# Kernel optimization log

Measured on AMD Instinct MI355X. Metric: run time of the kernel, lower is better.

## Reference

```python
import jax, jax.numpy as jnp
import numpy as np

B, S, D = 16, 2048, 64
SCALE = 1.0 / np.sqrt(np.float32(D))  # forward divides by sqrt(embedding_dim=64)


def setup_inputs() -> dict:
    key = jax.random.key(0)
    ks = jax.random.split(key, 7)
    return {
        "x": jax.random.normal(ks[0], (B, S, D), dtype=jnp.float32),
        "Wq": jax.random.normal(ks[1], (D, D), dtype=jnp.float32) * 0.02,
        "bq": jax.random.normal(ks[2], (D,), dtype=jnp.float32) * 0.02,
        "Wk": jax.random.normal(ks[3], (D, D), dtype=jnp.float32) * 0.02,
        "bk": jax.random.normal(ks[4], (D,), dtype=jnp.float32) * 0.02,
        "Wv": jax.random.normal(ks[5], (D, D), dtype=jnp.float32) * 0.02,
        "bv": jax.random.normal(ks[6], (D,), dtype=jnp.float32) * 0.02,
    }


def reference(x, Wq, bq, Wk, bk, Wv, bv):
    # Linear projections (weights stored [in, out], math-equivalent to nn.Linear)
    q = jnp.einsum("bsd,de->bse", x, Wq) + bq
    k = jnp.einsum("bsd,de->bse", x, Wk) + bk
    v = jnp.einsum("bsd,de->bse", x, Wv) + bv
    # Unfused scores: [B, S, S]
    scores = jnp.einsum("bqd,bkd->bqk", q, k) * jnp.float32(SCALE)
    causal = jnp.tril(jnp.ones((S, S), dtype=bool))  # mask[:S,:S]
    scores = jnp.where(causal, scores, jnp.float32(-jnp.inf))
    attn = jax.nn.softmax(scores, axis=-1)
    # dropout is identity in eval mode (reference baseline)
    out = jnp.einsum("bqk,bkd->bqd", attn, v)
    return out
```

## Files before the change

### kernel.cpp

```cpp
#include <hip/hip_runtime.h>

#define NB 16
#define SS 2048
#define DD 64

typedef __attribute__((ext_vector_type(8))) short short8;
typedef __attribute__((ext_vector_type(4))) float f32x4;

#define SCL2E 0.18033688011112042f

__device__ __forceinline__ short f2bf(float f) {
  union { float f; unsigned u; } v; v.f = f;
  unsigned r = (v.u + 0x7fffu + ((v.u >> 16) & 1u)) >> 16;
  return (short)r;
}

__device__ __forceinline__ unsigned cvtpk_bf16(float lo, float hi) {
  unsigned r;
  asm("v_cvt_pk_bf16_f32 %0, %1, %2" : "=v"(r) : "v"(lo), "v"(hi));
  return r;
}

__device__ __forceinline__ short8 load_a_frag_f32(const float* p) {
  float4 u = *(const float4*)p;
  float4 w = *(const float4*)(p + 4);
  short8 r;
  r[0] = f2bf(u.x); r[1] = f2bf(u.y); r[2] = f2bf(u.z); r[3] = f2bf(u.w);
  r[4] = f2bf(w.x); r[5] = f2bf(w.y); r[6] = f2bf(w.z); r[7] = f2bf(w.w);
  return r;
}

__global__ __launch_bounds__(256) void wprep_kernel(
    const float* __restrict__ Wq, const float* __restrict__ Wk,
    const float* __restrict__ Wv, ushort* __restrict__ Wt)
{
  const float* Ws[3] = {Wq, Wk, Wv};
  const int m = blockIdx.x;
  const float* src = Ws[m];
  ushort* dst = Wt + m * 4096;
  const int t = threadIdx.x;
#pragma unroll
  for (int i = 0; i < 4; ++i) {
    int idx = i * 1024 + t * 4;
    int k = idx >> 6, n0 = idx & 63;
    float4 w4 = *(const float4*)(src + idx);
    dst[(n0 + 0) * 64 + k] = (ushort)f2bf(w4.x);
    dst[(n0 + 1) * 64 + k] = (ushort)f2bf(w4.y);
    dst[(n0 + 2) * 64 + k] = (ushort)f2bf(w4.z);
    dst[(n0 + 3) * 64 + k] = (ushort)f2bf(w4.w);
  }
}

__global__ __launch_bounds__(256) void proj_kernel(
    const float* __restrict__ x, const ushort* __restrict__ Wt,
    const float* __restrict__ bq, const float* __restrict__ bk,
    const float* __restrict__ bv,
    ushort* __restrict__ qo, ushort* __restrict__ ko, ushort* __restrict__ vT)
{
  __shared__ __align__(16) ushort Vs[64][68];
  const int t = threadIdx.x;
  const int lane = t & 63, w = t >> 6;
  const int l15 = lane & 15, quad = lane >> 4;
  const int g = blockIdx.x * 64 + w * 16 + l15;
  short8 b0 = load_a_frag_f32(x + (size_t)g * 64 + quad * 8);
  short8 b1 = load_a_frag_f32(x + (size_t)g * 64 + 32 + quad * 8);
  const int lrow = w * 16 + l15;

#pragma unroll
  for (int m = 0; m < 3; ++m) {
    const float* bp = (m == 0 ? bq : (m == 1 ? bk : bv));
    const ushort* wm = Wt + m * 4096;
#pragma unroll
    for (int nt = 0; nt < 4; ++nt) {
      const ushort* ap = wm + (nt * 16 + l15) * 64 + quad * 8;
      short8 a0 = *(const short8*)ap;
      short8 a1 = *(const short8*)(ap + 32);
      f32x4 acc = {0.f, 0.f, 0.f, 0.f};
      acc = __builtin_amdgcn_mfma_f32_16x16x32_bf16(a0, b0, acc, 0, 0, 0);
      acc = __builtin_amdgcn_mfma_f32_16x16x32_bf16(a1, b1, acc, 0, 0, 0);
      float4 bb = *(const float4*)(bp + nt * 16 + quad * 4);
      unsigned p0 = cvtpk_bf16(acc[0] + bb.x, acc[1] + bb.y);
      unsigned p1 = cvtpk_bf16(acc[2] + bb.z, acc[3] + bb.w);
      uint2 pk; pk.x = p0; pk.y = p1;
      if (m == 0) {
        *(uint2*)(qo + (size_t)g * 64 + nt * 16 + quad * 4) = pk;
      } else if (m == 1) {
        *(uint2*)(ko + (size_t)g * 64 + nt * 16 + quad * 4) = pk;
      } else {
        *(uint2*)&Vs[lrow][nt * 16 + quad * 4] = pk;
      }
    }
  }
  __syncthreads();
  {
    const int batch = blockIdx.x >> 5;
    const int s0 = (blockIdx.x & 31) * 64;
    const int d = t >> 2, j0 = (t & 3) * 16;
    ushort tmp[16];
#pragma unroll
    for (int j = 0; j < 16; ++j) tmp[j] = Vs[j0 + j][d];
    ushort* dst = vT + (size_t)batch * DD * SS + (size_t)d * SS + s0 + j0;
    ((int4*)dst)[0] = ((int4*)tmp)[0];
    ((int4*)dst)[1] = ((int4*)tmp)[1];
  }
}

__device__ __forceinline__ short8 build_pa(unsigned A0, unsigned A1,
                                           unsigned B0, unsigned B1, int quad) {
  int xA0 = __shfl_xor((int)A0, 32);
  int xA1 = __shfl_xor((int)A1, 32);
  int xB0 = __shfl_xor((int)B0, 32);
  int xB1 = __shfl_xor((int)B1, 32);
  const bool hi = quad >= 2;
  const bool odd = quad & 1;
  int Lo0 = hi ? xB0 : (int)A0;
  int Lo1 = hi ? xB1 : (int)A1;
  int Hi0 = hi ? (int)B0 : xA0;
  int Hi1 = hi ? (int)B1 : xA1;
  int xLo0 = __shfl_xor(Lo0, 16);
  int xLo1 = __shfl_xor(Lo1, 16);
  int xHi0 = __shfl_xor(Hi0, 16);
  int xHi1 = __shfl_xor(Hi1, 16);
  int4 wv;
  wv.x = odd ? xHi0 : Lo0;
  wv.y = odd ? xHi1 : Lo1;
  wv.z = odd ? Hi0 : xLo0;
  wv.w = odd ? Hi1 : xLo1;
  return *(short8*)&wv;
}

template<bool MASKED>
__device__ __forceinline__ void attn_half(
    const f32x4 (&c)[4], float& l_acc, f32x4 (&acc)[4],
    const short8 (&vf0)[4], const short8 (&vf1)[4],
    int keybase, int qabs, int quad)
{
  unsigned pk[4][2];
#pragma unroll
  for (int ct = 0; ct < 4; ++ct) {
    float pe[4];
#pragma unroll
    for (int r = 0; r < 4; ++r) {
      float p = __builtin_amdgcn_exp2f(c[ct][r] * SCL2E);
      if (MASKED && (keybase + ct * 16 + quad * 4 + r > qabs)) p = 0.f;
      pe[r] = p;
      l_acc += p;
    }
    pk[ct][0] = cvtpk_bf16(pe[0], pe[1]);
    pk[ct][1] = cvtpk_bf16(pe[2], pe[3]);
  }
  short8 pa0 = build_pa(pk[0][0], pk[0][1], pk[1][0], pk[1][1], quad);
  short8 pa1 = build_pa(pk[2][0], pk[2][1], pk[3][0], pk[3][1], quad);
  __builtin_amdgcn_s_setprio(1);
#pragma unroll
  for (int nt = 0; nt < 4; ++nt) {
    acc[nt] = __builtin_amdgcn_mfma_f32_16x16x32_bf16(pa0, vf0[nt], acc[nt], 0, 0, 0);
    acc[nt] = __builtin_amdgcn_mfma_f32_16x16x32_bf16(pa1, vf1[nt], acc[nt], 0, 0, 0);
  }
  __builtin_amdgcn_s_setprio(0);
}

__global__ __launch_bounds__(256, 3) void attn_kernel(
    const ushort* __restrict__ qg, const ushort* __restrict__ kg,
    const ushort* __restrict__ vT, float* __restrict__ out)
{
  __shared__ __align__(16) float accW[4][32][68];
  __shared__ float lW[4][32];

  const int t = threadIdx.x, bid = blockIdx.x;
  const int batch = (bid & 7) * 2 + ((bid >> 3) & 1);
  const int qt = 63 - (bid >> 4);
  const int q0 = qt * 32;
  const int lane = t & 63, w = t >> 6;
  const int l15 = lane & 15, quad = lane >> 4;
  const size_t bbase = (size_t)batch * SS * DD;

  const ushort* qp = qg + bbase + (size_t)(q0 + l15) * 64 + quad * 8;
  short8 a0 = *(const short8*)qp;
  short8 a1 = *(const short8*)(qp + 32);
  short8 a2 = *(const short8*)(qp + 16 * 64);
  short8 a3 = *(const short8*)(qp + 16 * 64 + 32);

  f32x4 acc0[4], acc1[4];
  float l0 = 0.f, l1 = 0.f;
#pragma unroll
  for (int nt = 0; nt < 4; ++nt) {
    acc0[nt] = (f32x4){0.f, 0.f, 0.f, 0.f};
    acc1[nt] = (f32x4){0.f, 0.f, 0.f, 0.f};
  }

  const int ktotal = ((q0 + 31) >> 6) + 1;
  const ushort* kp0 = kg + bbase + (size_t)(w * 64 + l15) * 64 + quad * 8;
  const ushort* kp1 = kp0 + 2048;
  const ushort* vp0 = vT + bbase + (size_t)(l15) * SS + w * 64 + quad * 8;
  const ushort* vp1 = vp0 + 16 * SS;
  const ushort* vp2 = vp0 + 32 * SS;
  const ushort* vp3 = vp0 + 48 * SS;

  const int qabs0 = q0 + l15, qabs1 = q0 + 16 + l15;

  for (int kt = w; kt < ktotal; kt += 4) {
    short8 kf0[4], kf1[4], vf0[4], vf1[4];
    kf0[0] = *(const short8*)(kp0);
    kf1[0] = *(const short8*)(kp0 + 32);
    kf0[1] = *(const short8*)(kp0 + 1024);
    kf1[1] = *(const short8*)(kp0 + 1056);
    kf0[2] = *(const short8*)(kp1);
    kf1[2] = *(const short8*)(kp1 + 32);
    kf0[3] = *(const short8*)(kp1 + 1024);
    kf1[3] = *(const short8*)(kp1 + 1056);
    vf0[0] = *(const short8*)(vp0); vf1[0] = *(const short8*)(vp0 + 32);
    vf0[1] = *(const short8*)(vp1); vf1[1] = *(const short8*)(vp1 + 32);
    vf0[2] = *(const short8*)(vp2); vf1[2] = *(const short8*)(vp2 + 32);
    vf0[3] = *(const short8*)(vp3); vf1[3] = *(const short8*)(vp3 + 32);

    f32x4 c0[4], c1[4];
    __builtin_amdgcn_s_setprio(1);
#pragma unroll
    for (int ct = 0; ct < 4; ++ct) {
      f32x4 z = {0.f, 0.f, 0.f, 0.f};
      c0[ct] = __builtin_amdgcn_mfma_f32_16x16x32_bf16(kf0[ct], a0, z, 0, 0, 0);
      c0[ct] = __builtin_amdgcn_mfma_f32_16x16x32_bf16(kf1[ct], a1, c0[ct], 0, 0, 0);
      c1[ct] = __builtin_amdgcn_mfma_f32_16x16x32_bf16(kf0[ct], a2, z, 0, 0, 0);
      c1[ct] = __builtin_amdgcn_mfma_f32_16x16x32_bf16(kf1[ct], a3, c1[ct], 0, 0, 0);
    }
    __builtin_amdgcn_s_setprio(0);

    const int kb = kt * 64;
    if (kt == ktotal - 1) {
      attn_half<true >(c0, l0, acc0, vf0, vf1, kb, qabs0, quad);
      attn_half<true >(c1, l1, acc1, vf0, vf1, kb, qabs1, quad);
    } else {
      attn_half<false>(c0, l0, acc0, vf0, vf1, kb, qabs0, quad);
      attn_half<false>(c1, l1, acc1, vf0, vf1, kb, qabs1, quad);
    }
    kp0 += 16384; kp1 += 16384;
    vp0 += 256; vp1 += 256; vp2 += 256; vp3 += 256;
  }

  l0 += __shfl_xor(l0, 16); l0 += __shfl_xor(l0, 32);
  l1 += __shfl_xor(l1, 16); l1 += __shfl_xor(l1, 32);

#pragma unroll
  for (int r = 0; r < 4; ++r)
#pragma unroll
    for (int nt = 0; nt < 4; ++nt) {
      accW[w][quad * 4 + r][nt * 16 + l15] = acc0[nt][r];
      accW[w][16 + quad * 4 + r][nt * 16 + l15] = acc1[nt][r];
    }
  if (lane < 16) {
    lW[w][lane] = l0;
    lW[w][16 + lane] = l1;
  }
  __syncthreads();

  {
    const int row = t >> 3, col0 = (t & 7) * 8;
    float den = lW[0][row] + lW[1][row] + lW[2][row] + lW[3][row];
    float iv = 1.0f / den;
    float4 oa = {0.f, 0.f, 0.f, 0.f}, ob = {0.f, 0.f, 0.f, 0.f};
#pragma unroll
    for (int ww = 0; ww < 4; ++ww) {
      float4 x0 = *(const float4*)&accW[ww][row][col0];
      float4 x1 = *(const float4*)&accW[ww][row][col0 + 4];
      oa.x += x0.x; oa.y += x0.y; oa.z += x0.z; oa.w += x0.w;
      ob.x += x1.x; ob.y += x1.y; ob.z += x1.z; ob.w += x1.w;
    }
    oa.x *= iv; oa.y *= iv; oa.z *= iv; oa.w *= iv;
    ob.x *= iv; ob.y *= iv; ob.z *= iv; ob.w *= iv;
    float* op = out + bbase + (size_t)(q0 + row) * 64 + col0;
    *(float4*)op = oa;
    *(float4*)(op + 4) = ob;
  }
}

extern "C" void kernel_launch(void* const* d_in, const int* in_sizes, int n_in,
                              void* d_out, int out_size, void* d_ws, size_t ws_size,
                              hipStream_t stream) {
  (void)in_sizes; (void)n_in; (void)out_size; (void)ws_size;
  const float* x  = (const float*)d_in[0];
  const float* Wq = (const float*)d_in[1];
  const float* bq = (const float*)d_in[2];
  const float* Wk = (const float*)d_in[3];
  const float* bk = (const float*)d_in[4];
  const float* Wv = (const float*)d_in[5];
  const float* bv = (const float*)d_in[6];
  float* out = (float*)d_out;

  ushort* qws = (ushort*)d_ws;
  ushort* kws = qws + (size_t)NB * SS * DD;
  ushort* vws = kws + (size_t)NB * SS * DD;
  ushort* wt  = vws + (size_t)NB * SS * DD;

  wprep_kernel<<<dim3(3), dim3(256), 0, stream>>>(Wq, Wk, Wv, wt);
  proj_kernel<<<dim3(NB * SS / 64), dim3(256), 0, stream>>>(
      x, wt, bq, bk, bv, qws, kws, vws);
  attn_kernel<<<dim3(NB * (SS / 32)), dim3(256), 0, stream>>>(
      qws, kws, vws, out);
}
```

Measured before the change: 122.7 us.

## Halve attention query tile to 16 rows and split projection by matrix per wave

The attention kernel now gives each block 16 query rows instead of 32, which doubles the grid and raises the occupancy hint from 3 to 6. The aim is better load balance and latency hiding on the causal workload. Each block now reads its K/V tiles for only 16 query rows, so K/V traffic per unit of work roughly doubles. The projection kernel is reworked so each of 6 waves computes one of Q/K/V for 16 rows of a 32-row block, instead of each wave computing all three sequentially.

```diff
diff --git a/kernel.cpp b/kernel.cpp
--- a/kernel.cpp
+++ b/kernel.cpp
@@ -51,57 +51,54 @@
   }
 }
 
-__global__ __launch_bounds__(256) void proj_kernel(
+__global__ __launch_bounds__(384) void proj_kernel(
     const float* __restrict__ x, const ushort* __restrict__ Wt,
     const float* __restrict__ bq, const float* __restrict__ bk,
     const float* __restrict__ bv,
     ushort* __restrict__ qo, ushort* __restrict__ ko, ushort* __restrict__ vT)
 {
-  __shared__ __align__(16) ushort Vs[64][68];
+  __shared__ __align__(16) ushort Vs[32][68];
   const int t = threadIdx.x;
   const int lane = t & 63, w = t >> 6;
   const int l15 = lane & 15, quad = lane >> 4;
-  const int g = blockIdx.x * 64 + w * 16 + l15;
+  const int m = w >> 1, rh = w & 1;
+  const int g = blockIdx.x * 32 + rh * 16 + l15;
+
   short8 b0 = load_a_frag_f32(x + (size_t)g * 64 + quad * 8);
   short8 b1 = load_a_frag_f32(x + (size_t)g * 64 + 32 + quad * 8);
-  const int lrow = w * 16 + l15;
-
-#pragma unroll
-  for (int m = 0; m < 3; ++m) {
-    const float* bp = (m == 0 ? bq : (m == 1 ? bk : bv));
-    const ushort* wm = Wt + m * 4096;
-#pragma unroll
-    for (int nt = 0; nt < 4; ++nt) {
-      const ushort* ap = wm + (nt * 16 + l15) * 64 + quad * 8;
-      short8 a0 = *(const short8*)ap;
-      short8 a1 = *(const short8*)(ap + 32);
-      f32x4 acc = {0.f, 0.f, 0.f, 0.f};
-      acc = __builtin_amdgcn_mfma_f32_16x16x32_bf16(a0, b0, acc, 0, 0, 0);
-      acc = __builtin_amdgcn_mfma_f32_16x16x32_bf16(a1, b1, acc, 0, 0, 0);
-      float4 bb = *(const float4*)(bp + nt * 16 + quad * 4);
-      unsigned p0 = cvtpk_bf16(acc[0] + bb.x, acc[1] + bb.y);
-      unsigned p1 = cvtpk_bf16(acc[2] + bb.z, acc[3] + bb.w);
-      uint2 pk; pk.x = p0; pk.y = p1;
-      if (m == 0) {
-        *(uint2*)(qo + (size_t)g * 64 + nt * 16 + quad * 4) = pk;
-      } else if (m == 1) {
-        *(uint2*)(ko + (size_t)g * 64 + nt * 16 + quad * 4) = pk;
-      } else {
-        *(uint2*)&Vs[lrow][nt * 16 + quad * 4] = pk;
-      }
+
+  const float* bp = (m == 0 ? bq : (m == 1 ? bk : bv));
+  const ushort* wm = Wt + m * 4096;
+  ushort* outp = (m == 0 ? qo : ko);
+
+#pragma unroll
+  for (int nt = 0; nt < 4; ++nt) {
+    const ushort* ap = wm + (nt * 16 + l15) * 64 + quad * 8;
+    short8 a0 = *(const short8*)ap;
+    short8 a1 = *(const short8*)(ap + 32);
+    f32x4 acc = {0.f, 0.f, 0.f, 0.f};
+    acc = __builtin_amdgcn_mfma_f32_16x16x32_bf16(a0, b0, acc, 0, 0, 0);
+    acc = __builtin_amdgcn_mfma_f32_16x16x32_bf16(a1, b1, acc, 0, 0, 0);
+    float4 bb = *(const float4*)(bp + nt * 16 + quad * 4);
+    uint2 pk;
+    pk.x = cvtpk_bf16(acc[0] + bb.x, acc[1] + bb.y);
+    pk.y = cvtpk_bf16(acc[2] + bb.z, acc[3] + bb.w);
+    if (m == 2) {
+      *(uint2*)&Vs[rh * 16 + l15][nt * 16 + quad * 4] = pk;
+    } else {
+      *(uint2*)(outp + (size_t)g * 64 + nt * 16 + quad * 4) = pk;
     }
   }
   __syncthreads();
-  {
-    const int batch = blockIdx.x >> 5;
-    const int s0 = (blockIdx.x & 31) * 64;
-    const int d = t >> 2, j0 = (t & 3) * 16;
-    ushort tmp[16];
-#pragma unroll
-    for (int j = 0; j < 16; ++j) tmp[j] = Vs[j0 + j][d];
-    ushort* dst = vT + (size_t)batch * DD * SS + (size_t)d * SS + s0 + j0;
-    ((int4*)dst)[0] = ((int4*)tmp)[0];
-    ((int4*)dst)[1] = ((int4*)tmp)[1];
+  if (t < 256) {
+    const int batch = blockIdx.x >> 6;
+    const int s0 = (blockIdx.x & 63) * 32;
+    const int d = t >> 2, j0 = (t & 3) * 8;
+    ushort tmp[8];
+#pragma unroll
+    for (int j = 0; j < 8; ++j) tmp[j] = Vs[j0 + j][d];
+    *(int4*)(vT + (size_t)batch * DD * SS + (size_t)d * SS + s0 + j0) =
+        *(const int4*)tmp;
   }
 }
 
@@ -160,17 +157,17 @@
   __builtin_amdgcn_s_setprio(0);
 }
 
-__global__ __launch_bounds__(256, 3) void attn_kernel(
+__global__ __launch_bounds__(256, 6) void attn_kernel(
     const ushort* __restrict__ qg, const ushort* __restrict__ kg,
     const ushort* __restrict__ vT, float* __restrict__ out)
 {
-  __shared__ __align__(16) float accW[4][32][68];
-  __shared__ float lW[4][32];
+  __shared__ __align__(16) float accW[4][16][68];
+  __shared__ float lW[4][16];
 
   const int t = threadIdx.x, bid = blockIdx.x;
-  const int batch = (bid & 7) * 2 + ((bid >> 3) & 1);
-  const int qt = 63 - (bid >> 4);
-  const int q0 = qt * 32;
+  const int batch = bid & 15;
+  const int qt = 127 - (bid >> 4);
+  const int q0 = qt * 16;
   const int lane = t & 63, w = t >> 6;
   const int l15 = lane & 15, quad = lane >> 4;
   const size_t bbase = (size_t)batch * SS * DD;
@@ -178,18 +175,13 @@
   const ushort* qp = qg + bbase + (size_t)(q0 + l15) * 64 + quad * 8;
   short8 a0 = *(const short8*)qp;
   short8 a1 = *(const short8*)(qp + 32);
-  short8 a2 = *(const short8*)(qp + 16 * 64);
-  short8 a3 = *(const short8*)(qp + 16 * 64 + 32);
-
-  f32x4 acc0[4], acc1[4];
-  float l0 = 0.f, l1 = 0.f;
-#pragma unroll
-  for (int nt = 0; nt < 4; ++nt) {
-    acc0[nt] = (f32x4){0.f, 0.f, 0.f, 0.f};
-    acc1[nt] = (f32x4){0.f, 0.f, 0.f, 0.f};
-  }
-
-  const int ktotal = ((q0 + 31) >> 6) + 1;
+
+  f32x4 acc0[4];
+  float l0 = 0.f;
+#pragma unroll
+  for (int nt = 0; nt < 4; ++nt) acc0[nt] = (f32x4){0.f, 0.f, 0.f, 0.f};
+
+  const int ktotal = ((q0 + 15) >> 6) + 1;
   const ushort* kp0 = kg + bbase + (size_t)(w * 64 + l15) * 64 + quad * 8;
   const ushort* kp1 = kp0 + 2048;
   const ushort* vp0 = vT + bbase + (size_t)(l15) * SS + w * 64 + quad * 8;
@@ -197,7 +189,7 @@
   const ushort* vp2 = vp0 + 32 * SS;
   const ushort* vp3 = vp0 + 48 * SS;
 
-  const int qabs0 = q0 + l15, qabs1 = q0 + 16 + l15;
+  const int qabs0 = q0 + l15;
 
   for (int kt = w; kt < ktotal; kt += 4) {
     short8 kf0[4], kf1[4], vf0[4], vf1[4];
@@ -214,63 +206,48 @@
     vf0[2] = *(const short8*)(vp2); vf1[2] = *(const short8*)(vp2 + 32);
     vf0[3] = *(const short8*)(vp3); vf1[3] = *(const short8*)(vp3 + 32);
 
-    f32x4 c0[4], c1[4];
+    f32x4 c0[4];
     __builtin_amdgcn_s_setprio(1);
 #pragma unroll
     for (int ct = 0; ct < 4; ++ct) {
       f32x4 z = {0.f, 0.f, 0.f, 0.f};
       c0[ct] = __builtin_amdgcn_mfma_f32_16x16x32_bf16(kf0[ct], a0, z, 0, 0, 0);
       c0[ct] = __builtin_amdgcn_mfma_f32_16x16x32_bf16(kf1[ct], a1, c0[ct], 0, 0, 0);
-      c1[ct] = __builtin_amdgcn_mfma_f32_16x16x32_bf16(kf0[ct], a2, z, 0, 0, 0);
-      c1[ct] = __builtin_amdgcn_mfma_f32_16x16x32_bf16(kf1[ct], a3, c1[ct], 0, 0, 0);
     }
     __builtin_amdgcn_s_setprio(0);
 
     const int kb = kt * 64;
     if (kt == ktotal - 1) {
       attn_half<true >(c0, l0, acc0, vf0, vf1, kb, qabs0, quad);
-      attn_half<true >(c1, l1, acc1, vf0, vf1, kb, qabs1, quad);
     } else {
       attn_half<false>(c0, l0, acc0, vf0, vf1, kb, qabs0, quad);
-      attn_half<false>(c1, l1, acc1, vf0, vf1, kb, qabs1, quad);
     }
     kp0 += 16384; kp1 += 16384;
     vp0 += 256; vp1 += 256; vp2 += 256; vp3 += 256;
   }
 
   l0 += __shfl_xor(l0, 16); l0 += __shfl_xor(l0, 32);
-  l1 += __shfl_xor(l1, 16); l1 += __shfl_xor(l1, 32);
 
 #pragma unroll
   for (int r = 0; r < 4; ++r)
 #pragma unroll
-    for (int nt = 0; nt < 4; ++nt) {
+    for (int nt = 0; nt < 4; ++nt)
       accW[w][quad * 4 + r][nt * 16 + l15] = acc0[nt][r];
-      accW[w][16 + quad * 4 + r][nt * 16 + l15] = acc1[nt][r];
-    }
-  if (lane < 16) {
-    lW[w][lane] = l0;
-    lW[w][16 + lane] = l1;
-  }
+  if (lane < 16) lW[w][lane] = l0;
   __syncthreads();
 
   {
-    const int row = t >> 3, col0 = (t & 7) * 8;
+    const int row = t >> 4, col0 = (t & 15) * 4;
     float den = lW[0][row] + lW[1][row] + lW[2][row] + lW[3][row];
     float iv = 1.0f / den;
-    float4 oa = {0.f, 0.f, 0.f, 0.f}, ob = {0.f, 0.f, 0.f, 0.f};
+    float4 o = {0.f, 0.f, 0.f, 0.f};
 #pragma unroll
     for (int ww = 0; ww < 4; ++ww) {
       float4 x0 = *(const float4*)&accW[ww][row][col0];
-      float4 x1 = *(const float4*)&accW[ww][row][col0 + 4];
-      oa.x += x0.x; oa.y += x0.y; oa.z += x0.z; oa.w += x0.w;
-      ob.x += x1.x; ob.y += x1.y; ob.z += x1.z; ob.w += x1.w;
-    }
-    oa.x *= iv; oa.y *= iv; oa.z *= iv; oa.w *= iv;
-    ob.x *= iv; ob.y *= iv; ob.z *= iv; ob.w *= iv;
-    float* op = out + bbase + (size_t)(q0 + row) * 64 + col0;
-    *(float4*)op = oa;
-    *(float4*)(op + 4) = ob;
+      o.x += x0.x; o.y += x0.y; o.z += x0.z; o.w += x0.w;
+    }
+    o.x *= iv; o.y *= iv; o.z *= iv; o.w *= iv;
+    *(float4*)(out + bbase + (size_t)(q0 + row) * 64 + col0) = o;
   }
 }
 
@@ -293,8 +270,8 @@
   ushort* wt  = vws + (size_t)NB * SS * DD;
 
   wprep_kernel<<<dim3(3), dim3(256), 0, stream>>>(Wq, Wk, Wv, wt);
-  proj_kernel<<<dim3(NB * SS / 64), dim3(256), 0, stream>>>(
+  proj_kernel<<<dim3(NB * SS / 32), dim3(384), 0, stream>>>(
       x, wt, bq, bk, bv, qws, kws, vws);
-  attn_kernel<<<dim3(NB * (SS / 32)), dim3(256), 0, stream>>>(
+  attn_kernel<<<dim3(NB * (SS / 16)), dim3(256), 0, stream>>>(
       qws, kws, vws, out);
 }
```

New measurement: 191.8 us. 56.3% more time.

## Use 8 waves per attention block, tile V layout, split projection across grid

Applied to the files above, without the earlier changes.

The attention kernel now runs 512 threads (8 waves) per query tile, each wave taking every 8th key tile, and reduces partial accumulators through shared memory in two stages. V is stored in a tiled per-64-key layout so each wave reads contiguous 4096-element chunks instead of strided rows. The projection kernel gets a second grid dimension so Q, K and V are computed by separate blocks. The aim is more parallelism per query tile and better load locality, at the cost of an extra sync, a larger reduction and dropping the occupancy hint on launch bounds.

```diff
diff --git a/kernel.cpp b/kernel.cpp
--- a/kernel.cpp
+++ b/kernel.cpp
@@ -55,51 +55,49 @@
     const float* __restrict__ x, const ushort* __restrict__ Wt,
     const float* __restrict__ bq, const float* __restrict__ bk,
     const float* __restrict__ bv,
-    ushort* __restrict__ qo, ushort* __restrict__ ko, ushort* __restrict__ vT)
+    ushort* __restrict__ qo, ushort* __restrict__ ko, ushort* __restrict__ vt)
 {
   __shared__ __align__(16) ushort Vs[64][68];
   const int t = threadIdx.x;
   const int lane = t & 63, w = t >> 6;
   const int l15 = lane & 15, quad = lane >> 4;
-  const int g = blockIdx.x * 64 + w * 16 + l15;
+  const int rowgroup = blockIdx.x, mm = blockIdx.y;
+  const int g = rowgroup * 64 + w * 16 + l15;
+
   short8 b0 = load_a_frag_f32(x + (size_t)g * 64 + quad * 8);
   short8 b1 = load_a_frag_f32(x + (size_t)g * 64 + 32 + quad * 8);
-  const int lrow = w * 16 + l15;
-
-#pragma unroll
-  for (int m = 0; m < 3; ++m) {
-    const float* bp = (m == 0 ? bq : (m == 1 ? bk : bv));
-    const ushort* wm = Wt + m * 4096;
-#pragma unroll
-    for (int nt = 0; nt < 4; ++nt) {
-      const ushort* ap = wm + (nt * 16 + l15) * 64 + quad * 8;
-      short8 a0 = *(const short8*)ap;
-      short8 a1 = *(const short8*)(ap + 32);
-      f32x4 acc = {0.f, 0.f, 0.f, 0.f};
-      acc = __builtin_amdgcn_mfma_f32_16x16x32_bf16(a0, b0, acc, 0, 0, 0);
-      acc = __builtin_amdgcn_mfma_f32_16x16x32_bf16(a1, b1, acc, 0, 0, 0);
-      float4 bb = *(const float4*)(bp + nt * 16 + quad * 4);
-      unsigned p0 = cvtpk_bf16(acc[0] + bb.x, acc[1] + bb.y);
-      unsigned p1 = cvtpk_bf16(acc[2] + bb.z, acc[3] + bb.w);
-      uint2 pk; pk.x = p0; pk.y = p1;
-      if (m == 0) {
-        *(uint2*)(qo + (size_t)g * 64 + nt * 16 + quad * 4) = pk;
-      } else if (m == 1) {
-        *(uint2*)(ko + (size_t)g * 64 + nt * 16 + quad * 4) = pk;
-      } else {
-        *(uint2*)&Vs[lrow][nt * 16 + quad * 4] = pk;
-      }
-    }
-  }
-  __syncthreads();
-  {
-    const int batch = blockIdx.x >> 5;
-    const int s0 = (blockIdx.x & 31) * 64;
+
+  const float* bp = (mm == 0 ? bq : (mm == 1 ? bk : bv));
+  const ushort* wm = Wt + mm * 4096;
+  ushort* outp = (mm == 0 ? qo : ko);
+
+#pragma unroll
+  for (int nt = 0; nt < 4; ++nt) {
+    const ushort* ap = wm + (nt * 16 + l15) * 64 + quad * 8;
+    short8 a0 = *(const short8*)ap;
+    short8 a1 = *(const short8*)(ap + 32);
+    f32x4 acc = {0.f, 0.f, 0.f, 0.f};
+    acc = __builtin_amdgcn_mfma_f32_16x16x32_bf16(a0, b0, acc, 0, 0, 0);
+    acc = __builtin_amdgcn_mfma_f32_16x16x32_bf16(a1, b1, acc, 0, 0, 0);
+    float4 bb = *(const float4*)(bp + nt * 16 + quad * 4);
+    uint2 pk;
+    pk.x = cvtpk_bf16(acc[0] + bb.x, acc[1] + bb.y);
+    pk.y = cvtpk_bf16(acc[2] + bb.z, acc[3] + bb.w);
+    if (mm == 2) {
+      *(uint2*)&Vs[w * 16 + l15][nt * 16 + quad * 4] = pk;
+    } else {
+      *(uint2*)(outp + (size_t)g * 64 + nt * 16 + quad * 4) = pk;
+    }
+  }
+  if (mm == 2) {
+    __syncthreads();
+    const int batch = rowgroup >> 5;
+    const int ktile = rowgroup & 31;
     const int d = t >> 2, j0 = (t & 3) * 16;
     ushort tmp[16];
 #pragma unroll
     for (int j = 0; j < 16; ++j) tmp[j] = Vs[j0 + j][d];
-    ushort* dst = vT + (size_t)batch * DD * SS + (size_t)d * SS + s0 + j0;
+    ushort* dst = vt + (size_t)batch * SS * DD + ktile * 4096 + d * 64 + j0;
     ((int4*)dst)[0] = ((int4*)tmp)[0];
     ((int4*)dst)[1] = ((int4*)tmp)[1];
   }
@@ -160,12 +158,12 @@
   __builtin_amdgcn_s_setprio(0);
 }
 
-__global__ __launch_bounds__(256, 3) void attn_kernel(
+__global__ __launch_bounds__(512) void attn_kernel(
     const ushort* __restrict__ qg, const ushort* __restrict__ kg,
-    const ushort* __restrict__ vT, float* __restrict__ out)
+    const ushort* __restrict__ vt, float* __restrict__ out)
 {
   __shared__ __align__(16) float accW[4][32][68];
-  __shared__ float lW[4][32];
+  __shared__ float lW[8][32];
 
   const int t = threadIdx.x, bid = blockIdx.x;
   const int batch = (bid & 7) * 2 + ((bid >> 3) & 1);
@@ -192,14 +190,11 @@
   const int ktotal = ((q0 + 31) >> 6) + 1;
   const ushort* kp0 = kg + bbase + (size_t)(w * 64 + l15) * 64 + quad * 8;
   const ushort* kp1 = kp0 + 2048;
-  const ushort* vp0 = vT + bbase + (size_t)(l15) * SS + w * 64 + quad * 8;
-  const ushort* vp1 = vp0 + 16 * SS;
-  const ushort* vp2 = vp0 + 32 * SS;
-  const ushort* vp3 = vp0 + 48 * SS;
+  const ushort* vp = vt + bbase + w * 4096 + l15 * 64 + quad * 8;
 
   const int qabs0 = q0 + l15, qabs1 = q0 + 16 + l15;
 
-  for (int kt = w; kt < ktotal; kt += 4) {
+  for (int kt = w; kt < ktotal; kt += 8) {
     short8 kf0[4], kf1[4], vf0[4], vf1[4];
     kf0[0] = *(const short8*)(kp0);
     kf1[0] = *(const short8*)(kp0 + 32);
@@ -209,10 +204,10 @@
     kf1[2] = *(const short8*)(kp1 + 32);
     kf0[3] = *(const short8*)(kp1 + 1024);
     kf1[3] = *(const short8*)(kp1 + 1056);
-    vf0[0] = *(const short8*)(vp0); vf1[0] = *(const short8*)(vp0 + 32);
-    vf0[1] = *(const short8*)(vp1); vf1[1] = *(const short8*)(vp1 + 32);
-    vf0[2] = *(const short8*)(vp2); vf1[2] = *(const short8*)(vp2 + 32);
-    vf0[3] = *(const short8*)(vp3); vf1[3] = *(const short8*)(vp3 + 32);
+    vf0[0] = *(const short8*)(vp);         vf1[0] = *(const short8*)(vp + 32);
+    vf0[1] = *(const short8*)(vp + 1024);  vf1[1] = *(const short8*)(vp + 1056);
+    vf0[2] = *(const short8*)(vp + 2048);  vf1[2] = *(const short8*)(vp + 2080);
+    vf0[3] = *(const short8*)(vp + 3072);  vf1[3] = *(const short8*)(vp + 3104);
 
     f32x4 c0[4], c1[4];
     __builtin_amdgcn_s_setprio(1);
@@ -234,43 +229,50 @@
       attn_half<false>(c0, l0, acc0, vf0, vf1, kb, qabs0, quad);
       attn_half<false>(c1, l1, acc1, vf0, vf1, kb, qabs1, quad);
     }
-    kp0 += 16384; kp1 += 16384;
-    vp0 += 256; vp1 += 256; vp2 += 256; vp3 += 256;
+    kp0 += 32768; kp1 += 32768; vp += 32768;
   }
 
   l0 += __shfl_xor(l0, 16); l0 += __shfl_xor(l0, 32);
   l1 += __shfl_xor(l1, 16); l1 += __shfl_xor(l1, 32);
 
-#pragma unroll
-  for (int r = 0; r < 4; ++r)
-#pragma unroll
-    for (int nt = 0; nt < 4; ++nt) {
-      accW[w][quad * 4 + r][nt * 16 + l15] = acc0[nt][r];
-      accW[w][16 + quad * 4 + r][nt * 16 + l15] = acc1[nt][r];
-    }
   if (lane < 16) {
     lW[w][lane] = l0;
     lW[w][16 + lane] = l1;
   }
+  if (w < 4) {
+#pragma unroll
+    for (int r = 0; r < 4; ++r)
+#pragma unroll
+      for (int nt = 0; nt < 4; ++nt) {
+        accW[w][quad * 4 + r][nt * 16 + l15] = acc0[nt][r];
+        accW[w][16 + quad * 4 + r][nt * 16 + l15] = acc1[nt][r];
+      }
+  }
   __syncthreads();
+  if (w >= 4) {
+#pragma unroll
+    for (int r = 0; r < 4; ++r)
+#pragma unroll
+      for (int nt = 0; nt < 4; ++nt) {
+        accW[w - 4][quad * 4 + r][nt * 16 + l15] += acc0[nt][r];
+        accW[w - 4][16 + quad * 4 + r][nt * 16 + l15] += acc1[nt][r];
+      }
+  }
+  __syncthreads();
 
   {
-    const int row = t >> 3, col0 = (t & 7) * 8;
-    float den = lW[0][row] + lW[1][row] + lW[2][row] + lW[3][row];
+    const int row = t >> 4, col0 = (t & 15) * 4;
+    float den = lW[0][row] + lW[1][row] + lW[2][row] + lW[3][row] +
+                lW[4][row] + lW[5][row] + lW[6][row] + lW[7][row];
     float iv = 1.0f / den;
-    float4 oa = {0.f, 0.f, 0.f, 0.f}, ob = {0.f, 0.f, 0.f, 0.f};
+    float4 o = {0.f, 0.f, 0.f, 0.f};
 #pragma unroll
     for (int ww = 0; ww < 4; ++ww) {
       float4 x0 = *(const float4*)&accW[ww][row][col0];
-      float4 x1 = *(const float4*)&accW[ww][row][col0 + 4];
-      oa.x += x0.x; oa.y += x0.y; oa.z += x0.z; oa.w += x0.w;
-      ob.x += x1.x; ob.y += x1.y; ob.z += x1.z; ob.w += x1.w;
-    }
-    oa.x *= iv; oa.y *= iv; oa.z *= iv; oa.w *= iv;
-    ob.x *= iv; ob.y *= iv; ob.z *= iv; ob.w *= iv;
-    float* op = out + bbase + (size_t)(q0 + row) * 64 + col0;
-    *(float4*)op = oa;
-    *(float4*)(op + 4) = ob;
+      o.x += x0.x; o.y += x0.y; o.z += x0.z; o.w += x0.w;
+    }
+    o.x *= iv; o.y *= iv; o.z *= iv; o.w *= iv;
+    *(float4*)(out + bbase + (size_t)(q0 + row) * 64 + col0) = o;
   }
 }
 
@@ -293,8 +295,8 @@
   ushort* wt  = vws + (size_t)NB * SS * DD;
 
   wprep_kernel<<<dim3(3), dim3(256), 0, stream>>>(Wq, Wk, Wv, wt);
-  proj_kernel<<<dim3(NB * SS / 64), dim3(256), 0, stream>>>(
+  proj_kernel<<<dim3(512, 3), dim3(256), 0, stream>>>(
       x, wt, bq, bk, bv, qws, kws, vws);
-  attn_kernel<<<dim3(NB * (SS / 32)), dim3(256), 0, stream>>>(
+  attn_kernel<<<dim3(NB * (SS / 32)), dim3(512), 0, stream>>>(
       qws, kws, vws, out);
 }
```

New measurement: 130.3 us. 6.2% more time.
